# Optimization experiments

Measured on AMD Instinct MI355X. Metric: run time of the kernel, lower is better.

## Reference

```python
import jax, jax.numpy as jnp
import numpy as np

V, D, B, NEG, L = 100000, 128, 4096, 5, 6


def setup_inputs() -> dict:
    key = jax.random.key(0)
    ks = jax.random.split(key, 8)
    initrange = 0.5 / D
    return {
        "u_emb": jax.random.uniform(ks[0], (V, D), jnp.float32, -initrange, initrange),
        "v_emb": jax.random.uniform(ks[1], (V, D), jnp.float32, -initrange, initrange),
        "pos_u_idx": jax.random.randint(ks[2], (B, L), 0, V),
        "pos_u_len": jax.random.randint(ks[3], (B,), 0, L),
        "pos_v_idx": jax.random.randint(ks[4], (B, L), 0, V),
        "pos_v_len": jax.random.randint(ks[5], (B,), 0, L),
        "neg_v_idx": jax.random.randint(ks[6], (B * NEG, L), 0, V),
        "neg_v_len": jax.random.randint(ks[7], (B * NEG,), 0, L),
    }


def _mean_pool(table, idx, length):
    # ragged phrase mean-pool: actual lengths are length+1 in [1, L]
    n = (length + 1).astype(jnp.int32)                      # [M]
    mask = (jnp.arange(L)[None, :] < n[:, None])            # [M, L]
    emb = table[idx]                                        # [M, L, D]
    summed = jnp.sum(emb * mask[:, :, None].astype(table.dtype), axis=1)
    return summed / n[:, None].astype(table.dtype)          # [M, D]


def reference(u_emb, v_emb, pos_u_idx, pos_u_len, pos_v_idx, pos_v_len, neg_v_idx, neg_v_len):
    embed_u = _mean_pool(u_emb, pos_u_idx, pos_u_len)       # [B, D]
    embed_v = _mean_pool(v_emb, pos_v_idx, pos_v_len)       # [B, D]
    neg_embed_v = _mean_pool(v_emb, neg_v_idx, neg_v_len).reshape(B, NEG, D)

    score = jnp.sum(embed_u * embed_v, axis=1)              # [B]
    log_target = jax.nn.log_sigmoid(score)                  # [B]
    neg_score = jnp.einsum("bnd,bd->bn", neg_embed_v, embed_u)  # [B, NEG]
    sum_log_sampled = jnp.sum(jax.nn.log_sigmoid(-neg_score), axis=1)
    loss = log_target + sum_log_sampled
    return -jnp.sum(loss) / float(B)
```

## Files before the change

### kernel.cpp

```cpp
#include <hip/hip_runtime.h>

#define V_SZ 100000
#define D_SZ 128
#define B_SZ 4096
#define NEG_SZ 5
#define L_SZ 6

__device__ __forceinline__ float log_sigmoid(float x) {
    return fminf(x, 0.0f) - __logf(1.0f + __expf(-fabsf(x)));
}

__device__ __forceinline__ float wave_reduce_sum(float v) {
    #pragma unroll
    for (int off = 32; off > 0; off >>= 1) v += __shfl_xor(v, off);
    return v;
}

__global__ __launch_bounds__(256) void skipgram_loss_kernel(
    const float* __restrict__ u_emb,
    const float* __restrict__ v_emb,
    const int* __restrict__ pos_u_idx,
    const int* __restrict__ pos_u_len,
    const int* __restrict__ pos_v_idx,
    const int* __restrict__ pos_v_len,
    const int* __restrict__ neg_v_idx,
    const int* __restrict__ neg_v_len,
    float* __restrict__ per_b)
{
    __shared__ float lds[2][8][D_SZ];

    const int b0   = blockIdx.x * 2;
    const int wave = threadIdx.x >> 6;
    const int lane = threadIdx.x & 63;
    const int half = lane >> 5;
    const int dof  = (lane & 31) * 4;

    const int* idxp[4];
    const float* tab[4];
    int n[4], sb[4], sp[4];
    #pragma unroll
    for (int q = 0; q < 4; ++q) {
        const int bb = q >> 1;
        const int pp = wave + 4 * (q & 1);
        const int b  = b0 + bb;
        const int eff = (pp == 7) ? 3 : pp;
        sb[q] = bb; sp[q] = pp;
        if (eff == 0) {
            idxp[q] = pos_u_idx + b * L_SZ; tab[q] = u_emb; n[q] = pos_u_len[b] + 1;
        } else if (eff == 1) {
            idxp[q] = pos_v_idx + b * L_SZ; tab[q] = v_emb; n[q] = pos_v_len[b] + 1;
        } else {
            const int m = b * NEG_SZ + (eff - 2);
            idxp[q] = neg_v_idx + m * L_SZ; tab[q] = v_emb; n[q] = neg_v_len[m] + 1;
        }
        n[q] = __builtin_amdgcn_readfirstlane(n[q]);
    }

    int id[4][L_SZ];
    #pragma unroll
    for (int q = 0; q < 4; ++q)
        #pragma unroll
        for (int l = 0; l < L_SZ; ++l)
            id[q][l] = __builtin_amdgcn_readfirstlane(idxp[q][l]);

    float4 r[4][3];
    #pragma unroll
    for (int q = 0; q < 4; ++q)
        #pragma unroll
        for (int j = 0; j < 3; ++j) {
            const int idx = half ? id[q][2 * j + 1] : id[q][2 * j];
            r[q][j] = *reinterpret_cast<const float4*>(
                &tab[q][(size_t)idx * D_SZ + dof]);
        }

    #pragma unroll
    for (int q = 0; q < 4; ++q) {
        float4 a = make_float4(0.f, 0.f, 0.f, 0.f);
        #pragma unroll
        for (int j = 0; j < 3; ++j) {
            const bool valid = (2 * j + half) < n[q];
            a.x += valid ? r[q][j].x : 0.f;
            a.y += valid ? r[q][j].y : 0.f;
            a.z += valid ? r[q][j].z : 0.f;
            a.w += valid ? r[q][j].w : 0.f;
        }
        a.x += __shfl_xor(a.x, 32);
        a.y += __shfl_xor(a.y, 32);
        a.z += __shfl_xor(a.z, 32);
        a.w += __shfl_xor(a.w, 32);
        const float inv = 1.0f / (float)n[q];
        a.x *= inv; a.y *= inv; a.z *= inv; a.w *= inv;
        if (lane < 32)
            *reinterpret_cast<float4*>(&lds[sb[q]][sp[q]][dof]) = a;
    }
    __syncthreads();

    if (wave < 2) {
        const float2 eu = *reinterpret_cast<const float2*>(&lds[wave][0][2 * lane]);
        float s[6];
        #pragma unroll
        for (int k = 0; k < 6; ++k) {
            const float2 vp = *reinterpret_cast<const float2*>(
                &lds[wave][k + 1][2 * lane]);
            s[k] = eu.x * vp.x + eu.y * vp.y;
        }
        #pragma unroll
        for (int k = 0; k < 6; ++k) s[k] = wave_reduce_sum(s[k]);
        if (lane == 0) {
            float loss = log_sigmoid(s[0]);
            #pragma unroll
            for (int k = 1; k < 6; ++k) loss += log_sigmoid(-s[k]);
            per_b[b0 + wave] = loss;
        }
    }
}

__global__ __launch_bounds__(256) void skipgram_reduce_kernel(
    const float* __restrict__ per_b, float* __restrict__ out)
{
    __shared__ float s[4];
    float acc = 0.0f;
    #pragma unroll
    for (int i = 0; i < 4; ++i) {
        const float4 v = reinterpret_cast<const float4*>(per_b)[
            i * 256 + threadIdx.x];
        acc += (v.x + v.y) + (v.z + v.w);
    }
    acc = wave_reduce_sum(acc);
    const int wave = threadIdx.x >> 6;
    const int lane = threadIdx.x & 63;
    if (lane == 0) s[wave] = acc;
    __syncthreads();
    if (threadIdx.x == 0) {
        out[0] = -(s[0] + s[1] + s[2] + s[3]) / (float)B_SZ;
    }
}

extern "C" void kernel_launch(void* const* d_in, const int* in_sizes, int n_in,
                              void* d_out, int out_size, void* d_ws, size_t ws_size,
                              hipStream_t stream) {
    const float* u_emb     = (const float*)d_in[0];
    const float* v_emb     = (const float*)d_in[1];
    const int*   pos_u_idx = (const int*)d_in[2];
    const int*   pos_u_len = (const int*)d_in[3];
    const int*   pos_v_idx = (const int*)d_in[4];
    const int*   pos_v_len = (const int*)d_in[5];
    const int*   neg_v_idx = (const int*)d_in[6];
    const int*   neg_v_len = (const int*)d_in[7];
    float* out = (float*)d_out;

    float* per_b = (float*)d_ws;
    skipgram_loss_kernel<<<B_SZ / 2, 256, 0, stream>>>(
        u_emb, v_emb, pos_u_idx, pos_u_len, pos_v_idx, pos_v_len,
        neg_v_idx, neg_v_len, per_b);
    skipgram_reduce_kernel<<<1, 256, 0, stream>>>(per_b, out);
}
```

Before: 22.43 us.

## Fuse final reduction into loss kernel via fixed-point 64-bit atomic counters

Replaces the separate single-block reduce kernel with an in-kernel two-level atomic reduction. Each block packs its loss into a fixed-point value plus an arrival count, adds it to one of 64 slots, and the last arriving block in each slot forwards to a global slot whose last arrival writes the final output. A memset of the slots is still launched, so launch count may not shrink. The per-block loss is clamped at -31.9 to keep fixed-point packing within range, which changes results for extreme inputs. Lane mapping is also changed so that only 14 of 16 wave-slots do gathers, removing the duplicated negative gather.

```diff
diff --git a/kernel.cpp b/kernel.cpp
--- a/kernel.cpp
+++ b/kernel.cpp
@@ -6,6 +6,11 @@
 #define NEG_SZ 5
 #define L_SZ 6
 
+#define FXSCALE 137438953472.0
+#define BOFFSET 64.0
+#define MASK48  ((1ULL << 48) - 1)
+#define MASK56  ((1ULL << 56) - 1)
+
 __device__ __forceinline__ float log_sigmoid(float x) {
     return fminf(x, 0.0f) - __logf(1.0f + __expf(-fabsf(x)));
 }
@@ -16,7 +21,7 @@
     return v;
 }
 
-__global__ __launch_bounds__(256) void skipgram_loss_kernel(
+__global__ __launch_bounds__(256) void skipgram_fused_kernel(
     const float* __restrict__ u_emb,
     const float* __restrict__ v_emb,
     const int* __restrict__ pos_u_idx,
@@ -25,9 +30,11 @@
     const int* __restrict__ pos_v_len,
     const int* __restrict__ neg_v_idx,
     const int* __restrict__ neg_v_len,
-    float* __restrict__ per_b)
+    unsigned long long* __restrict__ slots,
+    float* __restrict__ out)
 {
-    __shared__ float lds[2][8][D_SZ];
+    __shared__ float lds[2][7][D_SZ];
+    __shared__ float loss_pair[2];
 
     const int b0   = blockIdx.x * 2;
     const int wave = threadIdx.x >> 6;
@@ -38,20 +45,23 @@
     const int* idxp[4];
     const float* tab[4];
     int n[4], sb[4], sp[4];
+    bool act[4];
     #pragma unroll
     for (int q = 0; q < 4; ++q) {
-        const int bb = q >> 1;
-        const int pp = wave + 4 * (q & 1);
+        const int m = wave + 4 * q;
+        act[q] = (m < 14);
+        const int mm = act[q] ? m : 0;
+        const int bb = mm / 7;
+        const int pp = mm % 7;
         const int b  = b0 + bb;
-        const int eff = (pp == 7) ? 3 : pp;
         sb[q] = bb; sp[q] = pp;
-        if (eff == 0) {
+        if (pp == 0) {
             idxp[q] = pos_u_idx + b * L_SZ; tab[q] = u_emb; n[q] = pos_u_len[b] + 1;
-        } else if (eff == 1) {
+        } else if (pp == 1) {
             idxp[q] = pos_v_idx + b * L_SZ; tab[q] = v_emb; n[q] = pos_v_len[b] + 1;
         } else {
-            const int m = b * NEG_SZ + (eff - 2);
-            idxp[q] = neg_v_idx + m * L_SZ; tab[q] = v_emb; n[q] = neg_v_len[m] + 1;
+            const int m2 = b * NEG_SZ + (pp - 2);
+            idxp[q] = neg_v_idx + m2 * L_SZ; tab[q] = v_emb; n[q] = neg_v_len[m2] + 1;
         }
         n[q] = __builtin_amdgcn_readfirstlane(n[q]);
     }
@@ -90,7 +100,7 @@
         a.w += __shfl_xor(a.w, 32);
         const float inv = 1.0f / (float)n[q];
         a.x *= inv; a.y *= inv; a.z *= inv; a.w *= inv;
-        if (lane < 32)
+        if (act[q] && lane < 32)
             *reinterpret_cast<float4*>(&lds[sb[q]][sp[q]][dof]) = a;
     }
     __syncthreads();
@@ -110,29 +120,102 @@
             float loss = log_sigmoid(s[0]);
             #pragma unroll
             for (int k = 1; k < 6; ++k) loss += log_sigmoid(-s[k]);
-            per_b[b0 + wave] = loss;
-        }
-    }
-}
-
-__global__ __launch_bounds__(256) void skipgram_reduce_kernel(
-    const float* __restrict__ per_b, float* __restrict__ out)
+            loss_pair[wave] = fmaxf(loss, -31.9f);
+        }
+    }
+    __syncthreads();
+
+    if (threadIdx.x == 0) {
+        const float bl = loss_pair[0] + loss_pair[1];
+        const unsigned long long pack =
+            (1ULL << 48) +
+            (unsigned long long)llrint(((double)bl + BOFFSET) * FXSCALE);
+        const unsigned long long old1 = atomicAdd(&slots[blockIdx.x & 63], pack);
+        if ((old1 >> 48) == 31) {
+            const unsigned long long v1 = (old1 + pack) & MASK48;
+            const unsigned long long pack2 = (1ULL << 56) + v1;
+            const unsigned long long old2 = atomicAdd(&slots[64], pack2);
+            if ((old2 >> 56) == 63) {
+                const unsigned long long tot = (old2 + pack2) & MASK56;
+                const double sum_loss =
+                    (double)tot / FXSCALE - BOFFSET * (double)(B_SZ / 2);
+                out[0] = (float)(-sum_loss / (double)B_SZ);
+            }
+        }
+    }
+}
+
+__global__ __launch_bounds__(256) void skipgram_atomic_fallback(
+    const float* __restrict__ u_emb,
+    const float* __restrict__ v_emb,
+    const int* __restrict__ pos_u_idx,
+    const int* __restrict__ pos_u_len,
+    const int* __restrict__ pos_v_idx,
+    const int* __restrict__ pos_v_len,
+    const int* __restrict__ neg_v_idx,
+    const int* __restrict__ neg_v_len,
+    float* __restrict__ out)
 {
-    __shared__ float s[4];
-    float acc = 0.0f;
-    #pragma unroll
-    for (int i = 0; i < 4; ++i) {
-        const float4 v = reinterpret_cast<const float4*>(per_b)[
-            i * 256 + threadIdx.x];
-        acc += (v.x + v.y) + (v.z + v.w);
-    }
-    acc = wave_reduce_sum(acc);
     const int wave = threadIdx.x >> 6;
     const int lane = threadIdx.x & 63;
-    if (lane == 0) s[wave] = acc;
-    __syncthreads();
-    if (threadIdx.x == 0) {
-        out[0] = -(s[0] + s[1] + s[2] + s[3]) / (float)B_SZ;
+    const int b    = blockIdx.x * 4 + wave;
+    const int half = lane >> 5;
+    const int dof  = (lane & 31) * 4;
+
+    int n[7];
+    n[0] = pos_u_len[b] + 1;
+    n[1] = pos_v_len[b] + 1;
+    #pragma unroll
+    for (int k = 0; k < NEG_SZ; ++k) n[2 + k] = neg_v_len[b * NEG_SZ + k] + 1;
+    int id[7][L_SZ];
+    #pragma unroll
+    for (int l = 0; l < L_SZ; ++l) id[0][l] = pos_u_idx[b * L_SZ + l];
+    #pragma unroll
+    for (int l = 0; l < L_SZ; ++l) id[1][l] = pos_v_idx[b * L_SZ + l];
+    #pragma unroll
+    for (int k = 0; k < NEG_SZ; ++k)
+        #pragma unroll
+        for (int l = 0; l < L_SZ; ++l)
+            id[2 + k][l] = neg_v_idx[(b * NEG_SZ + k) * L_SZ + l];
+
+    float4 a[7];
+    #pragma unroll
+    for (int p = 0; p < 7; ++p) {
+        const float* t = (p == 0) ? u_emb : v_emb;
+        float4 acc = make_float4(0.f, 0.f, 0.f, 0.f);
+        #pragma unroll
+        for (int j = 0; j < 3; ++j) {
+            const int idx = half ? id[p][2 * j + 1] : id[p][2 * j];
+            const float4 r = *reinterpret_cast<const float4*>(
+                &t[(size_t)idx * D_SZ + dof]);
+            const bool valid = (2 * j + half) < n[p];
+            acc.x += valid ? r.x : 0.f;
+            acc.y += valid ? r.y : 0.f;
+            acc.z += valid ? r.z : 0.f;
+            acc.w += valid ? r.w : 0.f;
+        }
+        acc.x += __shfl_xor(acc.x, 32);
+        acc.y += __shfl_xor(acc.y, 32);
+        acc.z += __shfl_xor(acc.z, 32);
+        acc.w += __shfl_xor(acc.w, 32);
+        const float inv = 1.0f / (float)n[p];
+        acc.x *= inv; acc.y *= inv; acc.z *= inv; acc.w *= inv;
+        a[p] = acc;
+    }
+    float s[6];
+    #pragma unroll
+    for (int k = 0; k < 6; ++k)
+        s[k] = a[0].x * a[k + 1].x + a[0].y * a[k + 1].y +
+               a[0].z * a[k + 1].z + a[0].w * a[k + 1].w;
+    #pragma unroll
+    for (int k = 0; k < 6; ++k)
+        #pragma unroll
+        for (int off = 16; off > 0; off >>= 1) s[k] += __shfl_xor(s[k], off);
+    if (lane == 0) {
+        float loss = log_sigmoid(s[0]);
+        #pragma unroll
+        for (int k = 1; k < 6; ++k) loss += log_sigmoid(-s[k]);
+        atomicAdd(out, -loss / (float)B_SZ);
     }
 }
 
@@ -149,9 +232,17 @@
     const int*   neg_v_len = (const int*)d_in[7];
     float* out = (float*)d_out;
 
-    float* per_b = (float*)d_ws;
-    skipgram_loss_kernel<<<B_SZ / 2, 256, 0, stream>>>(
-        u_emb, v_emb, pos_u_idx, pos_u_len, pos_v_idx, pos_v_len,
-        neg_v_idx, neg_v_len, per_b);
-    skipgram_reduce_kernel<<<1, 256, 0, stream>>>(per_b, out);
-}
+    const size_t need = 65 * sizeof(unsigned long long);
+    if (ws_size >= need) {
+        unsigned long long* slots = (unsigned long long*)d_ws;
+        hipMemsetAsync(d_ws, 0, need, stream);
+        skipgram_fused_kernel<<<B_SZ / 2, 256, 0, stream>>>(
+            u_emb, v_emb, pos_u_idx, pos_u_len, pos_v_idx, pos_v_len,
+            neg_v_idx, neg_v_len, slots, out);
+    } else {
+        hipMemsetAsync(d_out, 0, sizeof(float), stream);
+        skipgram_atomic_fallback<<<B_SZ / 4, 256, 0, stream>>>(
+            u_emb, v_emb, pos_u_idx, pos_u_len, pos_v_idx, pos_v_len,
+            neg_v_idx, neg_v_len, out);
+    }
+}
```

Measured after the change: 28.21 us. 1.26x slower.
